# Kernel tuning notes

Hardware: AMD Instinct MI355X
Metric: run time of the kernel (lower is better)

The kernel has to match this reference:

```python
import jax, jax.numpy as jnp
import numpy as np


def setup_inputs() -> dict:
    key = jax.random.key(0)
    k1, k2, k3, k4 = jax.random.split(key, 4)
    M, K, N, G = 4, 8192, 28672, 128
    x = jax.random.normal(k1, (M, K), dtype=jnp.float16)
    # packed uint4 pairs stored as bytes (values 0..255); int32 carrier dtype
    weight_packed = jax.random.randint(k2, (K // 2, N), 0, 256, dtype=jnp.int32)
    # small positive scales, typical of int4 quant
    scales = (jax.random.uniform(k3, (K // G, N), dtype=jnp.float16) * 0.02 + 0.001).astype(jnp.float16)
    bias = jax.random.normal(k4, (N,), dtype=jnp.float16)
    return {"x": x, "weight_packed": weight_packed, "scales": scales, "bias": bias, "group_size": G}


def _dequant(weight_packed, scales, group_size):
    # weight_packed: [K//2, N] bytes; low nibble = even k, high nibble = odd k
    half_K, N = weight_packed.shape
    K = 2 * half_K
    low = weight_packed & 0xF
    high = (weight_packed >> 4) & 0xF
    w = jnp.stack([low, high], axis=1).reshape(K, N)  # interleave along K
    deq = w.astype(jnp.float16) - jnp.float16(8.0)     # symmetric int4, zero-point 8
    # per-group scale along K: scales is [K//group_size, N]
    deq = (deq.reshape(K // group_size, group_size, N) * scales[:, None, :]).reshape(K, N)
    return deq


def reference(x, weight_packed, scales, bias, group_size):
    deq = _dequant(weight_packed, scales, group_size)  # [K, N] fp16
    out = jnp.einsum('mk,kn->mn', x, deq, preferred_element_type=jnp.float32)
    out = out.astype(jnp.float16)
    return out + bias
```

## Files before the change

kernel.cpp:

```cpp
#include <hip/hip_runtime.h>
#include <stdint.h>

#define M_DIM 4
#define K_DIM 8192
#define N_DIM 28672
#define GRP 128
#define KK_TOTAL (K_DIM / 2)
#define KK_PER_GRP (GRP / 2)
#define N_GROUPS (K_DIM / GRP)
#define BLOCK 256
#define COLS_PER_THREAD 4
#define COLS_PER_BLOCK (BLOCK * COLS_PER_THREAD)
#define NBLK (N_DIM / COLS_PER_BLOCK)


__global__ __launch_bounds__(BLOCK) void int4_gemv_main(
    const float* __restrict__ x,
    const int*   __restrict__ wp,
    const float* __restrict__ scales,
    float*       __restrict__ ws,
    int gps)
{
    __shared__ float xs[GRP * M_DIM];

    const int tid   = threadIdx.x;
    const int nb    = blockIdx.x;
    const int split = blockIdx.y;
    const int g0    = split * gps;
    const int n0    = nb * COLS_PER_BLOCK + tid * COLS_PER_THREAD;

    float acc[M_DIM][COLS_PER_THREAD];
    #pragma unroll
    for (int m = 0; m < M_DIM; m++)
        #pragma unroll
        for (int c = 0; c < COLS_PER_THREAD; c++) acc[m][c] = 0.f;

    for (int gi = 0; gi < gps; gi++) {
        const int g = g0 + gi;

        __syncthreads();
        for (int e = tid; e < GRP * M_DIM; e += BLOCK) {
            const int m = e & 3;
            const int j = e >> 2;
            xs[e] = x[m * K_DIM + g * GRP + j];
        }
        __syncthreads();

        const float4 sv = *(const float4*)(scales + (size_t)g * N_DIM + n0);
        const float s[COLS_PER_THREAD] = {sv.x, sv.y, sv.z, sv.w};

        float accg[M_DIM][COLS_PER_THREAD];
        #pragma unroll
        for (int m = 0; m < M_DIM; m++)
            #pragma unroll
            for (int c = 0; c < COLS_PER_THREAD; c++) accg[m][c] = 0.f;

        const int* wrow = wp + (size_t)(g * KK_PER_GRP) * N_DIM + n0;

        #pragma unroll 4
        for (int kkl = 0; kkl < KK_PER_GRP; kkl++) {
            const int4 w4 = *(const int4*)(wrow + (size_t)kkl * N_DIM);

            float xl[M_DIM], xh[M_DIM];
            #pragma unroll
            for (int m = 0; m < M_DIM; m++) {
                xl[m] = xs[(2 * kkl) * M_DIM + m];
                xh[m] = xs[(2 * kkl + 1) * M_DIM + m];
            }

            const int wv[4] = {w4.x, w4.y, w4.z, w4.w};
            #pragma unroll
            for (int c = 0; c < COLS_PER_THREAD; c++) {
                const float lo = (float)(wv[c] & 0xF) - 8.0f;
                const float hi = (float)((wv[c] >> 4) & 0xF) - 8.0f;
                #pragma unroll
                for (int m = 0; m < M_DIM; m++) {
                    accg[m][c] = fmaf(xl[m], lo, accg[m][c]);
                    accg[m][c] = fmaf(xh[m], hi, accg[m][c]);
                }
            }
        }

        #pragma unroll
        for (int m = 0; m < M_DIM; m++)
            #pragma unroll
            for (int c = 0; c < COLS_PER_THREAD; c++)
                acc[m][c] = fmaf(accg[m][c], s[c], acc[m][c]);
    }

    float* wsp = ws + (size_t)split * (M_DIM * N_DIM);
    #pragma unroll
    for (int m = 0; m < M_DIM; m++) {
        float4 v = make_float4(acc[m][0], acc[m][1], acc[m][2], acc[m][3]);
        *(float4*)(wsp + (size_t)m * N_DIM + n0) = v;
    }
}

__global__ __launch_bounds__(256) void int4_gemv_reduce(
    const float* __restrict__ ws,
    const float* __restrict__ bias,
    float*       __restrict__ out,
    int splits)
{
    const int idx = blockIdx.x * 256 + threadIdx.x;
    if (idx >= M_DIM * N_DIM) return;
    const int n = idx % N_DIM;
    float a = bias[n];
    for (int s = 0; s < splits; s++)
        a += ws[(size_t)s * (M_DIM * N_DIM) + idx];
    out[idx] = a;
}

extern "C" void kernel_launch(void* const* d_in, const int* in_sizes, int n_in,
                              void* d_out, int out_size, void* d_ws, size_t ws_size,
                              hipStream_t stream) {
    const float* x      = (const float*)d_in[0];
    const int*   wpk    = (const int*)d_in[1];
    const float* scales = (const float*)d_in[2];
    const float* bias   = (const float*)d_in[3];

    float* out = (float*)d_out;
    float* ws  = (float*)d_ws;

    int splits = N_GROUPS;
    while (splits > 1 &&
           (size_t)splits * (size_t)(M_DIM * N_DIM) * sizeof(float) > ws_size)
        splits >>= 1;
    const int gps = N_GROUPS / splits;

    dim3 grid(NBLK, splits);
    int4_gemv_main<<<grid, BLOCK, 0, stream>>>(x, wpk, scales, ws, gps);

    const int total = M_DIM * N_DIM;
    int4_gemv_reduce<<<(total + 255) / 256, 256, 0, stream>>>(ws, bias, out, splits);
}
```

Baseline: 637.1 us.

## Add fast one-group-per-block int4 GEMV path with register prefetch and vectorized reduce

Adds a fast path, used when the workspace can hold all 64 group partials. Each block handles one quantization group and 8 columns per thread, prefetches weight rows into registers four deep, and reads x as float4 from a transposed shared-memory layout. Scales are applied once at the end instead of per group, and a float4-vectorized reduce kernel sums the 64 partials plus bias. The old split-K kernel is kept as a fallback when the workspace is too small. The cost is more register pressure and a larger workspace write and read in the reduce.

```diff
diff --git a/kernel.cpp b/kernel.cpp
--- a/kernel.cpp
+++ b/kernel.cpp
@@ -5,74 +5,163 @@
 #define K_DIM 8192
 #define N_DIM 28672
 #define GRP 128
-#define KK_TOTAL (K_DIM / 2)
 #define KK_PER_GRP (GRP / 2)
 #define N_GROUPS (K_DIM / GRP)
 #define BLOCK 256
-#define COLS_PER_THREAD 4
-#define COLS_PER_BLOCK (BLOCK * COLS_PER_THREAD)
-#define NBLK (N_DIM / COLS_PER_BLOCK)
-
-
-__global__ __launch_bounds__(BLOCK) void int4_gemv_main(
+
+#define CPT 8
+#define COLS_PER_BLOCK (BLOCK * CPT)
+#define NBLK_FAST (N_DIM / COLS_PER_BLOCK)
+#define PF 4
+
+
+__global__ __launch_bounds__(BLOCK, 4) void int4_gemv_fast(
     const float* __restrict__ x,
     const int*   __restrict__ wp,
     const float* __restrict__ scales,
-    float*       __restrict__ ws,
-    int gps)
+    float*       __restrict__ ws)
 {
     __shared__ float xs[GRP * M_DIM];
 
-    const int tid   = threadIdx.x;
-    const int nb    = blockIdx.x;
+    const int tid = threadIdx.x;
+    const int g   = blockIdx.y;
+    const int n0  = blockIdx.x * COLS_PER_BLOCK + tid * CPT;
+
+    #pragma unroll
+    for (int e = tid; e < GRP * M_DIM; e += BLOCK) {
+        const int m = e >> 7;
+        const int j = e & 127;
+        xs[j * M_DIM + m] = x[m * K_DIM + g * GRP + j];
+    }
+    __syncthreads();
+
+    float acc[M_DIM][CPT];
+    #pragma unroll
+    for (int m = 0; m < M_DIM; m++)
+        #pragma unroll
+        for (int c = 0; c < CPT; c++) acc[m][c] = 0.f;
+
+    const int* wrow = wp + (size_t)g * KK_PER_GRP * N_DIM + n0;
+
+    int4 bufA[PF], bufB[PF];
+    #pragma unroll
+    for (int i = 0; i < PF; i++) {
+        bufA[i] = *(const int4*)(wrow + (size_t)i * N_DIM);
+        bufB[i] = *(const int4*)(wrow + (size_t)i * N_DIM + 4);
+    }
+
+    #pragma unroll 4
+    for (int kk = 0; kk < KK_PER_GRP; kk++) {
+        const int cur = kk & (PF - 1);
+        const int4 wa = bufA[cur];
+        const int4 wb = bufB[cur];
+        if (kk + PF < KK_PER_GRP) {
+            bufA[cur] = *(const int4*)(wrow + (size_t)(kk + PF) * N_DIM);
+            bufB[cur] = *(const int4*)(wrow + (size_t)(kk + PF) * N_DIM + 4);
+        }
+
+        const float4 xlo = *(const float4*)&xs[(2 * kk) * M_DIM];
+        const float4 xhi = *(const float4*)&xs[(2 * kk + 1) * M_DIM];
+
+        const int wv[CPT] = {wa.x, wa.y, wa.z, wa.w, wb.x, wb.y, wb.z, wb.w};
+        #pragma unroll
+        for (int c = 0; c < CPT; c++) {
+            const float lo = (float)(wv[c] & 0xF) - 8.0f;
+            const float hi = (float)(wv[c] >> 4) - 8.0f;
+            acc[0][c] = fmaf(xlo.x, lo, acc[0][c]);
+            acc[1][c] = fmaf(xlo.y, lo, acc[1][c]);
+            acc[2][c] = fmaf(xlo.z, lo, acc[2][c]);
+            acc[3][c] = fmaf(xlo.w, lo, acc[3][c]);
+            acc[0][c] = fmaf(xhi.x, hi, acc[0][c]);
+            acc[1][c] = fmaf(xhi.y, hi, acc[1][c]);
+            acc[2][c] = fmaf(xhi.z, hi, acc[2][c]);
+            acc[3][c] = fmaf(xhi.w, hi, acc[3][c]);
+        }
+    }
+
+    const float4 s0 = *(const float4*)(scales + (size_t)g * N_DIM + n0);
+    const float4 s1 = *(const float4*)(scales + (size_t)g * N_DIM + n0 + 4);
+    const float sc[CPT] = {s0.x, s0.y, s0.z, s0.w, s1.x, s1.y, s1.z, s1.w};
+
+    float* wsp = ws + (size_t)g * (M_DIM * N_DIM);
+    #pragma unroll
+    for (int m = 0; m < M_DIM; m++) {
+        float4 o0 = make_float4(acc[m][0] * sc[0], acc[m][1] * sc[1],
+                                acc[m][2] * sc[2], acc[m][3] * sc[3]);
+        float4 o1 = make_float4(acc[m][4] * sc[4], acc[m][5] * sc[5],
+                                acc[m][6] * sc[6], acc[m][7] * sc[7]);
+        *(float4*)(wsp + (size_t)m * N_DIM + n0)     = o0;
+        *(float4*)(wsp + (size_t)m * N_DIM + n0 + 4) = o1;
+    }
+}
+
+__global__ __launch_bounds__(256) void int4_gemv_reduce64(
+    const float* __restrict__ ws,
+    const float* __restrict__ bias,
+    float*       __restrict__ out)
+{
+    const int mn = (blockIdx.x * 256 + threadIdx.x) * 4;
+    if (mn >= M_DIM * N_DIM) return;
+    const int n = mn % N_DIM;
+    float4 a = *(const float4*)(bias + n);
+    #pragma unroll 8
+    for (int s = 0; s < N_GROUPS; s++) {
+        const float4 v = *(const float4*)(ws + (size_t)s * (M_DIM * N_DIM) + mn);
+        a.x += v.x; a.y += v.y; a.z += v.z; a.w += v.w;
+    }
+    *(float4*)(out + mn) = a;
+}
+
+#define G_CPT 4
+#define G_COLS_PER_BLOCK (BLOCK * G_CPT)
+#define G_NBLK (N_DIM / G_COLS_PER_BLOCK)
+
+__global__ __launch_bounds__(BLOCK) void int4_gemv_generic(
+    const float* __restrict__ x, const int* __restrict__ wp,
+    const float* __restrict__ scales, float* __restrict__ ws, int gps)
+{
+    __shared__ float xs[GRP * M_DIM];
+    const int tid = threadIdx.x;
     const int split = blockIdx.y;
-    const int g0    = split * gps;
-    const int n0    = nb * COLS_PER_BLOCK + tid * COLS_PER_THREAD;
-
-    float acc[M_DIM][COLS_PER_THREAD];
+    const int g0 = split * gps;
+    const int n0 = blockIdx.x * G_COLS_PER_BLOCK + tid * G_CPT;
+
+    float acc[M_DIM][G_CPT];
     #pragma unroll
     for (int m = 0; m < M_DIM; m++)
         #pragma unroll
-        for (int c = 0; c < COLS_PER_THREAD; c++) acc[m][c] = 0.f;
+        for (int c = 0; c < G_CPT; c++) acc[m][c] = 0.f;
 
     for (int gi = 0; gi < gps; gi++) {
         const int g = g0 + gi;
-
         __syncthreads();
         for (int e = tid; e < GRP * M_DIM; e += BLOCK) {
-            const int m = e & 3;
-            const int j = e >> 2;
+            const int m = e & 3, j = e >> 2;
             xs[e] = x[m * K_DIM + g * GRP + j];
         }
         __syncthreads();
-
         const float4 sv = *(const float4*)(scales + (size_t)g * N_DIM + n0);
-        const float s[COLS_PER_THREAD] = {sv.x, sv.y, sv.z, sv.w};
-
-        float accg[M_DIM][COLS_PER_THREAD];
+        const float s[G_CPT] = {sv.x, sv.y, sv.z, sv.w};
+        float accg[M_DIM][G_CPT];
         #pragma unroll
         for (int m = 0; m < M_DIM; m++)
             #pragma unroll
-            for (int c = 0; c < COLS_PER_THREAD; c++) accg[m][c] = 0.f;
-
+            for (int c = 0; c < G_CPT; c++) accg[m][c] = 0.f;
         const int* wrow = wp + (size_t)(g * KK_PER_GRP) * N_DIM + n0;
-
         #pragma unroll 4
         for (int kkl = 0; kkl < KK_PER_GRP; kkl++) {
             const int4 w4 = *(const int4*)(wrow + (size_t)kkl * N_DIM);
-
             float xl[M_DIM], xh[M_DIM];
             #pragma unroll
             for (int m = 0; m < M_DIM; m++) {
                 xl[m] = xs[(2 * kkl) * M_DIM + m];
                 xh[m] = xs[(2 * kkl + 1) * M_DIM + m];
             }
-
             const int wv[4] = {w4.x, w4.y, w4.z, w4.w};
             #pragma unroll
-            for (int c = 0; c < COLS_PER_THREAD; c++) {
+            for (int c = 0; c < G_CPT; c++) {
                 const float lo = (float)(wv[c] & 0xF) - 8.0f;
-                const float hi = (float)((wv[c] >> 4) & 0xF) - 8.0f;
+                const float hi = (float)(wv[c] >> 4) - 8.0f;
                 #pragma unroll
                 for (int m = 0; m < M_DIM; m++) {
                     accg[m][c] = fmaf(xl[m], lo, accg[m][c]);
@@ -80,27 +169,22 @@
                 }
             }
         }
-
         #pragma unroll
         for (int m = 0; m < M_DIM; m++)
             #pragma unroll
-            for (int c = 0; c < COLS_PER_THREAD; c++)
+            for (int c = 0; c < G_CPT; c++)
                 acc[m][c] = fmaf(accg[m][c], s[c], acc[m][c]);
     }
-
     float* wsp = ws + (size_t)split * (M_DIM * N_DIM);
     #pragma unroll
-    for (int m = 0; m < M_DIM; m++) {
-        float4 v = make_float4(acc[m][0], acc[m][1], acc[m][2], acc[m][3]);
-        *(float4*)(wsp + (size_t)m * N_DIM + n0) = v;
-    }
-}
-
-__global__ __launch_bounds__(256) void int4_gemv_reduce(
-    const float* __restrict__ ws,
-    const float* __restrict__ bias,
-    float*       __restrict__ out,
-    int splits)
+    for (int m = 0; m < M_DIM; m++)
+        *(float4*)(wsp + (size_t)m * N_DIM + n0) =
+            make_float4(acc[m][0], acc[m][1], acc[m][2], acc[m][3]);
+}
+
+__global__ __launch_bounds__(256) void int4_gemv_reduce_generic(
+    const float* __restrict__ ws, const float* __restrict__ bias,
+    float* __restrict__ out, int splits)
 {
     const int idx = blockIdx.x * 256 + threadIdx.x;
     if (idx >= M_DIM * N_DIM) return;
@@ -118,19 +202,24 @@
     const int*   wpk    = (const int*)d_in[1];
     const float* scales = (const float*)d_in[2];
     const float* bias   = (const float*)d_in[3];
-
     float* out = (float*)d_out;
     float* ws  = (float*)d_ws;
 
-    int splits = N_GROUPS;
-    while (splits > 1 &&
-           (size_t)splits * (size_t)(M_DIM * N_DIM) * sizeof(float) > ws_size)
-        splits >>= 1;
-    const int gps = N_GROUPS / splits;
-
-    dim3 grid(NBLK, splits);
-    int4_gemv_main<<<grid, BLOCK, 0, stream>>>(x, wpk, scales, ws, gps);
-
-    const int total = M_DIM * N_DIM;
-    int4_gemv_reduce<<<(total + 255) / 256, 256, 0, stream>>>(ws, bias, out, splits);
-}
+    const size_t need = (size_t)N_GROUPS * (M_DIM * N_DIM) * sizeof(float);
+    if (ws_size >= need) {
+        dim3 grid(NBLK_FAST, N_GROUPS);
+        int4_gemv_fast<<<grid, BLOCK, 0, stream>>>(x, wpk, scales, ws);
+        int4_gemv_reduce64<<<(M_DIM * N_DIM / 4 + 255) / 256, 256, 0, stream>>>(
+            ws, bias, out);
+    } else {
+        int splits = N_GROUPS;
+        while (splits > 1 &&
+               (size_t)splits * (size_t)(M_DIM * N_DIM) * sizeof(float) > ws_size)
+            splits >>= 1;
+        const int gps = N_GROUPS / splits;
+        dim3 grid(G_NBLK, splits);
+        int4_gemv_generic<<<grid, BLOCK, 0, stream>>>(x, wpk, scales, ws, gps);
+        int4_gemv_reduce_generic<<<(M_DIM * N_DIM + 255) / 256, 256, 0, stream>>>(
+            ws, bias, out, splits);
+    }
+}
```

Result: no change. 630.8 us (-1.0%).

## Replace split-K workspace reduction with per-group atomic accumulation and register prefetch

Applied to the files above, without the earlier changes.

Removes the workspace-plus-reduce kernel. A small kernel now initialises the output with bias, and the main kernel runs one block per (column tile, K group) and adds its scaled partial sums straight into the output with float atomics. Each thread now handles 8 columns, keeps a software prefetch ring of 4 weight rows in registers, and reads x from a transposed shared layout as float4. This avoids writing and re-reading a large split-K workspace, but it adds many atomics per output element and the float sum order is no longer deterministic.

```diff
diff --git a/kernel.cpp b/kernel.cpp
--- a/kernel.cpp
+++ b/kernel.cpp
@@ -5,110 +5,100 @@
 #define K_DIM 8192
 #define N_DIM 28672
 #define GRP 128
-#define KK_TOTAL (K_DIM / 2)
 #define KK_PER_GRP (GRP / 2)
 #define N_GROUPS (K_DIM / GRP)
 #define BLOCK 256
-#define COLS_PER_THREAD 4
-#define COLS_PER_BLOCK (BLOCK * COLS_PER_THREAD)
-#define NBLK (N_DIM / COLS_PER_BLOCK)
+
+#define CPT 8
+#define COLS_PER_BLOCK (BLOCK * CPT)
+#define NBLK_FAST (N_DIM / COLS_PER_BLOCK)
+#define PF 4
 
 
-__global__ __launch_bounds__(BLOCK) void int4_gemv_main(
+__global__ __launch_bounds__(256) void bias_init(
+    const float* __restrict__ bias, float* __restrict__ out)
+{
+    const int i = (blockIdx.x * 256 + threadIdx.x) * 4;
+    if (i >= M_DIM * N_DIM) return;
+    const int n = i % N_DIM;
+    *(float4*)(out + i) = *(const float4*)(bias + n);
+}
+
+__global__ __launch_bounds__(BLOCK, 4) void int4_gemv_fast_atomic(
     const float* __restrict__ x,
     const int*   __restrict__ wp,
     const float* __restrict__ scales,
-    float*       __restrict__ ws,
-    int gps)
+    float*       __restrict__ out)
 {
     __shared__ float xs[GRP * M_DIM];
 
-    const int tid   = threadIdx.x;
-    const int nb    = blockIdx.x;
-    const int split = blockIdx.y;
-    const int g0    = split * gps;
-    const int n0    = nb * COLS_PER_BLOCK + tid * COLS_PER_THREAD;
+    const int tid = threadIdx.x;
+    const int g   = blockIdx.y;
+    const int n0  = blockIdx.x * COLS_PER_BLOCK + tid * CPT;
 
-    float acc[M_DIM][COLS_PER_THREAD];
+    #pragma unroll
+    for (int e = tid; e < GRP * M_DIM; e += BLOCK) {
+        const int m = e >> 7;
+        const int j = e & 127;
+        xs[j * M_DIM + m] = x[m * K_DIM + g * GRP + j];
+    }
+    __syncthreads();
+
+    float acc[M_DIM][CPT];
     #pragma unroll
     for (int m = 0; m < M_DIM; m++)
         #pragma unroll
-        for (int c = 0; c < COLS_PER_THREAD; c++) acc[m][c] = 0.f;
+        for (int c = 0; c < CPT; c++) acc[m][c] = 0.f;
 
-    for (int gi = 0; gi < gps; gi++) {
-        const int g = g0 + gi;
+    const int* wrow = wp + (size_t)g * KK_PER_GRP * N_DIM + n0;
 
-        __syncthreads();
-        for (int e = tid; e < GRP * M_DIM; e += BLOCK) {
-            const int m = e & 3;
-            const int j = e >> 2;
-            xs[e] = x[m * K_DIM + g * GRP + j];
-        }
-        __syncthreads();
+    int4 bufA[PF], bufB[PF];
+    #pragma unroll
+    for (int i = 0; i < PF; i++) {
+        bufA[i] = *(const int4*)(wrow + (size_t)i * N_DIM);
+        bufB[i] = *(const int4*)(wrow + (size_t)i * N_DIM + 4);
+    }
 
-        const float4 sv = *(const float4*)(scales + (size_t)g * N_DIM + n0);
-        const float s[COLS_PER_THREAD] = {sv.x, sv.y, sv.z, sv.w};
-
-        float accg[M_DIM][COLS_PER_THREAD];
-        #pragma unroll
-        for (int m = 0; m < M_DIM; m++)
-            #pragma unroll
-            for (int c = 0; c < COLS_PER_THREAD; c++) accg[m][c] = 0.f;
-
-        const int* wrow = wp + (size_t)(g * KK_PER_GRP) * N_DIM + n0;
-
-        #pragma unroll 4
-        for (int kkl = 0; kkl < KK_PER_GRP; kkl++) {
-            const int4 w4 = *(const int4*)(wrow + (size_t)kkl * N_DIM);
-
-            float xl[M_DIM], xh[M_DIM];
-            #pragma unroll
-            for (int m = 0; m < M_DIM; m++) {
-                xl[m] = xs[(2 * kkl) * M_DIM + m];
-                xh[m] = xs[(2 * kkl + 1) * M_DIM + m];
-            }
-
-            const int wv[4] = {w4.x, w4.y, w4.z, w4.w};
-            #pragma unroll
-            for (int c = 0; c < COLS_PER_THREAD; c++) {
-                const float lo = (float)(wv[c] & 0xF) - 8.0f;
-                const float hi = (float)((wv[c] >> 4) & 0xF) - 8.0f;
-                #pragma unroll
-                for (int m = 0; m < M_DIM; m++) {
-                    accg[m][c] = fmaf(xl[m], lo, accg[m][c]);
-                    accg[m][c] = fmaf(xh[m], hi, accg[m][c]);
-                }
-            }
+    #pragma unroll 4
+    for (int kk = 0; kk < KK_PER_GRP; kk++) {
+        const int cur = kk & (PF - 1);
+        const int4 wa = bufA[cur];
+        const int4 wb = bufB[cur];
+        if (kk + PF < KK_PER_GRP) {
+            bufA[cur] = *(const int4*)(wrow + (size_t)(kk + PF) * N_DIM);
+            bufB[cur] = *(const int4*)(wrow + (size_t)(kk + PF) * N_DIM + 4);
         }
 
+        const float4 xlo = *(const float4*)&xs[(2 * kk) * M_DIM];
+        const float4 xhi = *(const float4*)&xs[(2 * kk + 1) * M_DIM];
+
+        const int wv[CPT] = {wa.x, wa.y, wa.z, wa.w, wb.x, wb.y, wb.z, wb.w};
         #pragma unroll
-        for (int m = 0; m < M_DIM; m++)
-            #pragma unroll
-            for (int c = 0; c < COLS_PER_THREAD; c++)
-                acc[m][c] = fmaf(accg[m][c], s[c], acc[m][c]);
+        for (int c = 0; c < CPT; c++) {
+            const float lo = (float)(wv[c] & 0xF) - 8.0f;
+            const float hi = (float)(wv[c] >> 4) - 8.0f;
+            acc[0][c] = fmaf(xlo.x, lo, acc[0][c]);
+            acc[1][c] = fmaf(xlo.y, lo, acc[1][c]);
+            acc[2][c] = fmaf(xlo.z, lo, acc[2][c]);
+            acc[3][c] = fmaf(xlo.w, lo, acc[3][c]);
+            acc[0][c] = fmaf(xhi.x, hi, acc[0][c]);
+            acc[1][c] = fmaf(xhi.y, hi, acc[1][c]);
+            acc[2][c] = fmaf(xhi.z, hi, acc[2][c]);
+            acc[3][c] = fmaf(xhi.w, hi, acc[3][c]);
+        }
     }
 
-    float* wsp = ws + (size_t)split * (M_DIM * N_DIM);
+    const float4 s0 = *(const float4*)(scales + (size_t)g * N_DIM + n0);
+    const float4 s1 = *(const float4*)(scales + (size_t)g * N_DIM + n0 + 4);
+    const float sc[CPT] = {s0.x, s0.y, s0.z, s0.w, s1.x, s1.y, s1.z, s1.w};
+
     #pragma unroll
     for (int m = 0; m < M_DIM; m++) {
-        float4 v = make_float4(acc[m][0], acc[m][1], acc[m][2], acc[m][3]);
-        *(float4*)(wsp + (size_t)m * N_DIM + n0) = v;
+        float* op = out + (size_t)m * N_DIM + n0;
+        #pragma unroll
+        for (int c = 0; c < CPT; c++)
+            atomicAdd(op + c, acc[m][c] * sc[c]);
     }
-}
-
-__global__ __launch_bounds__(256) void int4_gemv_reduce(
-    const float* __restrict__ ws,
-    const float* __restrict__ bias,
-    float*       __restrict__ out,
-    int splits)
-{
-    const int idx = blockIdx.x * 256 + threadIdx.x;
-    if (idx >= M_DIM * N_DIM) return;
-    const int n = idx % N_DIM;
-    float a = bias[n];
-    for (int s = 0; s < splits; s++)
-        a += ws[(size_t)s * (M_DIM * N_DIM) + idx];
-    out[idx] = a;
 }
 
 extern "C" void kernel_launch(void* const* d_in, const int* in_sizes, int n_in,
@@ -118,19 +108,11 @@
     const int*   wpk    = (const int*)d_in[1];
     const float* scales = (const float*)d_in[2];
     const float* bias   = (const float*)d_in[3];
+    float* out = (float*)d_out;
+    (void)d_ws; (void)ws_size;
 
-    float* out = (float*)d_out;
-    float* ws  = (float*)d_ws;
+    bias_init<<<(M_DIM * N_DIM / 4 + 255) / 256, 256, 0, stream>>>(bias, out);
 
-    int splits = N_GROUPS;
-    while (splits > 1 &&
-           (size_t)splits * (size_t)(M_DIM * N_DIM) * sizeof(float) > ws_size)
-        splits >>= 1;
-    const int gps = N_GROUPS / splits;
-
-    dim3 grid(NBLK, splits);
-    int4_gemv_main<<<grid, BLOCK, 0, stream>>>(x, wpk, scales, ws, gps);
-
-    const int total = M_DIM * N_DIM;
-    int4_gemv_reduce<<<(total + 255) / 256, 256, 0, stream>>>(ws, bias, out, splits);
+    dim3 grid(NBLK_FAST, N_GROUPS);
+    int4_gemv_fast_atomic<<<grid, BLOCK, 0, stream>>>(x, wpk, scales, out);
 }
```

Measured after the change: 781.2 us. 1.23x slower.
